# Optimization experiments

Measured on AMD Instinct MI355X. Metric: run time of the kernel, lower is better.

The kernel has to match this reference:

```python
import jax, jax.numpy as jnp
import numpy as np

N, E, G, NH, H = 50000, 400000, 1024, 64, 1
EPS = 1e-5

def _bn(x):
    # BatchNorm1d in training mode, affine at init (gamma=1, beta=0), biased var
    m = x.mean(0)
    v = ((x - m) ** 2).mean(0)
    return (x - m) * jax.lax.rsqrt(v + EPS)

def _seg_softmax(logits, seg, num_segments):
    # numerically stable per-segment softmax (torch_geometric.utils.softmax)
    mx = jax.ops.segment_max(logits, seg, num_segments=num_segments)
    e = jnp.exp(logits - mx[seg])
    s = jax.ops.segment_sum(e, seg, num_segments=num_segments)
    return e / s[seg]

def setup_inputs() -> dict:
    key = jax.random.key(0)
    ks = jax.random.split(key, 16)
    p = lambda k, shape, s=0.1: jax.random.normal(k, shape, jnp.float32) * s
    return {
        "x": jax.random.normal(ks[0], (N, 92), jnp.float32),
        "edge_index": jax.random.randint(ks[1], (2, E), 0, N),
        "edge_attr": jax.random.normal(ks[2], (E, 41), jnp.float32),
        "batch": jnp.sort(jax.random.randint(ks[3], (N,), 0, G)),
        "global_feat": jax.random.normal(ks[4], (G, 103), jnp.float32),
        "emb_n_W": p(ks[5], (92, NH)), "emb_n_b": jnp.zeros((NH,), jnp.float32),
        "emb_e_W": p(ks[6], (41, NH)), "emb_e_b": jnp.zeros((NH,), jnp.float32),
        "conv_W": p(ks[7], (3, 2 * NH, H * NH)),
        "conv_att": p(ks[8], (3, H, 2 * NH)),
        "conv_bias": jnp.zeros((3, H * NH), jnp.float32),
        "comp_node_W": p(ks[9], (NH + 103, 32)), "comp_node_b": jnp.zeros((32,), jnp.float32),
        "comp_att_W": p(ks[10], (32, 1)), "comp_att_b": jnp.zeros((1,), jnp.float32),
        "fc_W": p(ks[11], (NH, 1)), "fc_b": jnp.zeros((1,), jnp.float32),
    }

def reference(x, edge_index, edge_attr, batch, global_feat,
              emb_n_W, emb_n_b, emb_e_W, emb_e_b,
              conv_W, conv_att, conv_bias,
              comp_node_W, comp_node_b, comp_att_W, comp_att_b,
              fc_W, fc_b):
    sp = jax.nn.softplus
    src, dst = edge_index[0], edge_index[1]  # PyG: x_j = x[src], aggregate by dst
    h = x @ emb_n_W + emb_n_b                              # [N, NH]
    ea = jax.nn.leaky_relu(edge_attr @ emb_e_W + emb_e_b, 0.2)  # [E, NH]
    for l in range(3):  # AGATConv layers
        hi = jnp.concatenate([h[dst], ea], -1)             # [E, 2*NH]
        hj = jnp.concatenate([h[src], ea], -1)
        ti = sp(hi @ conv_W[l]).reshape(E, H, NH)
        tj = sp(hj @ conv_W[l]).reshape(E, H, NH)
        alpha = sp(jnp.sum(jnp.concatenate([ti, tj], -1) * conv_att[l][None], -1))  # [E, H]
        alpha = sp(_bn(alpha))
        alpha = _seg_softmax(alpha, dst, N)                # segment softmax per dst node
        agg = jax.ops.segment_sum(tj * alpha[..., None], dst, num_segments=N)  # [N, H, NH]
        h = agg.reshape(N, H * NH) + conv_bias[l]
        h = sp(_bn(h))                                     # outer BatchNorm1d + softplus
    # composition attention: repeat_interleave(global_feat, counts) == gather by graph id
    gf = global_feat[batch]                                # [N, 103]
    a = sp(jnp.concatenate([h, gf], -1) @ comp_node_W + comp_node_b) @ comp_att_W + comp_att_b
    w = _seg_softmax(a, batch, G)                          # [N, 1]
    pooled = jax.ops.segment_sum(h * w, batch, num_segments=G)  # global_add_pool
    return pooled @ fc_W + fc_b                            # [G, 1]
```

## Files before the change

### kernel.cpp

```cpp
#include <hip/hip_runtime.h>
#include <hip/hip_bf16.h>
#include <hip/hip_fp16.h>
#include <math.h>


typedef unsigned short ushortt;
typedef _Float16 half2v __attribute__((ext_vector_type(2)));

__device__ __forceinline__ float sp_f(float x) {
  return x > 20.0f ? x : __logf(1.0f + __expf(x));
}
__device__ __forceinline__ float h2f(ushortt u) {
  union { ushortt u; __half h; } c; c.u = u;
  return __half2float(c.h);
}
__device__ __forceinline__ ushortt f2h(float f) {
  union { __half h; ushortt u; } c; c.h = __float2half(f);
  return c.u;
}
__device__ __forceinline__ float4 h4_to_f4(ushort4 u) {
  return make_float4(h2f(u.x), h2f(u.y), h2f(u.z), h2f(u.w));
}
__device__ __forceinline__ unsigned pack2h(float a, float b) {
  union { _Float16 h[2]; unsigned u; } c;
  c.h[0] = (_Float16)a; c.h[1] = (_Float16)b;
  return c.u;
}
__device__ __forceinline__ float fdot2f(unsigned a, unsigned b, float c) {
  return __builtin_amdgcn_fdot2(__builtin_bit_cast(half2v, a),
                                __builtin_bit_cast(half2v, b), c, false);
}

#define SLOTS 2304

template<int K, int ACT, int BIAS, int FUSE_A, int LH16, int GATHER, int FUSE_BN,
         typename IT, typename OT>
__global__ __launch_bounds__(256) void k_gemm_rt(
    const IT* __restrict__ in, const float* __restrict__ W,
    const float* __restrict__ b, OT* __restrict__ out, int R,
    const int* __restrict__ rows, const ushortt* __restrict__ P,
    const int* __restrict__ srcp, const int* __restrict__ dstp,
    const float* __restrict__ catt, float* __restrict__ a1,
    float* __restrict__ stats, const float* __restrict__ csbn, float invN)
{
  constexpr int KP  = (K + 3) / 4 * 4;
  constexpr int LSf = KP + 4;
  constexpr int LSb = K + 8;
  constexpr size_t INS_B = LH16 ? (size_t)64 * LSb * 2 : (size_t)64 * LSf * 4;
  constexpr size_t WS_B  = LH16 ? (size_t)(K / 2) * 64 * 4 : (size_t)KP * 64 * 4;
  __shared__ __align__(16) unsigned char smem[INS_B + WS_B];
  __shared__ float atts[128];
  __shared__ float ssum[4], ssq[4];
  __shared__ float bnm[64], bns[64];
  ushortt*  insb = (ushortt*)smem;
  unsigned* Wp   = (unsigned*)(smem + INS_B);
  float*    insf = (float*)smem;
  float*    Wsf  = (float*)(smem + INS_B);

  const int tx = threadIdx.x;
  const int b0 = blockIdx.x * 64;

  if (FUSE_BN) {
    if (tx < 64) {
      float mn = 0.f, sq = 0.f;
      #pragma unroll
      for (int bk = 0; bk < 16; ++bk) {
        mn += csbn[bk * 128 + tx];
        sq += csbn[bk * 128 + 64 + tx];
      }
      mn *= invN; sq *= invN;
      bnm[tx] = mn;
      bns[tx] = rsqrtf(sq - mn * mn + 1e-5f);
    }
    __syncthreads();
  }

  if (LH16) {
    static_assert(!LH16 || (K % 8 == 0), "fp16 path needs K%8==0");
    for (int i = tx; i < (K / 2) * 64; i += 256) {
      const int k2 = i >> 6;
      const int c = i & 63;
      Wp[i] = pack2h(W[(2 * k2) * 64 + c], W[(2 * k2 + 1) * 64 + c]);
    }
    for (int i = tx; i < 64 * (K / 8); i += 256) {
      const int row = i / (K / 8);
      const int k8 = i % (K / 8);
      long r = b0 + row; if (r >= R) r = R - 1;
      if (GATHER) r = rows[r];
      *(uint4*)&insb[row * LSb + k8 * 8] =
          *(const uint4*)&((const ushortt*)in)[r * (long)K + k8 * 8];
    }
  } else {
    for (int i = tx; i < KP * 64; i += 256) {
      const int k = i >> 6;
      Wsf[i] = (k < K) ? W[i] : 0.0f;
    }
    for (int i = tx; i < 64 * (KP / 4); i += 256) {
      const int row = i / (KP / 4);
      const int k4 = i % (KP / 4);
      long r = b0 + row; if (r >= R) r = R - 1;
      if (GATHER) r = rows[r];
      float4 v;
      if (K % 4 == 0) {
        v = *(const float4*)&((const float*)in)[r * (long)K + k4 * 4];
      } else {
        float t[4];
        #pragma unroll
        for (int j = 0; j < 4; ++j) {
          const int k = k4 * 4 + j;
          t[j] = (k < K) ? ((const float*)in)[r * (long)K + k] : 0.0f;
        }
        v = make_float4(t[0], t[1], t[2], t[3]);
      }
      if (FUSE_BN) {
        float* vv = (float*)&v;
        #pragma unroll
        for (int j = 0; j < 4; ++j) {
          const int c = k4 * 4 + j;
          vv[j] = sp_f((vv[j] - bnm[c]) * bns[c]);
        }
      }
      *(float4*)&insf[row * LSf + k4 * 4] = v;
    }
  }
  if (FUSE_A) { if (tx < 128) atts[tx] = catt[tx]; }
  __syncthreads();

  const int lr0 = ((tx >> 6) << 4) + (((tx >> 4) & 3) << 2);
  const int c0 = (tx & 15) << 2;

  ushort4 pdv[4], psv[4];
  if (FUSE_A) {
    #pragma unroll
    for (int ri = 0; ri < 4; ++ri) {
      long e = b0 + lr0 + ri; if (e >= R) e = R - 1;
      const int s = srcp[e];
      const int d = dstp[e];
      psv[ri] = *(const ushort4*)&P[(long)s * 64 + c0];
      pdv[ri] = *(const ushort4*)&P[(long)d * 64 + c0];
    }
  }

  float acc[4][4];
  #pragma unroll
  for (int i = 0; i < 4; ++i)
    #pragma unroll
    for (int j = 0; j < 4; ++j) acc[i][j] = 0.0f;

  if (LH16) {
    #pragma unroll 1
    for (int k8 = 0; k8 < K / 8; ++k8) {
      const uint4 wv0 = *(const uint4*)&Wp[(k8 * 4 + 0) * 64 + c0];
      const uint4 wv1 = *(const uint4*)&Wp[(k8 * 4 + 1) * 64 + c0];
      const uint4 wv2 = *(const uint4*)&Wp[(k8 * 4 + 2) * 64 + c0];
      const uint4 wv3 = *(const uint4*)&Wp[(k8 * 4 + 3) * 64 + c0];
      #pragma unroll
      for (int ri = 0; ri < 4; ++ri) {
        const uint4 av = *(const uint4*)&insb[(lr0 + ri) * LSb + k8 * 8];
        acc[ri][0] = fdot2f(av.x, wv0.x, acc[ri][0]);
        acc[ri][1] = fdot2f(av.x, wv0.y, acc[ri][1]);
        acc[ri][2] = fdot2f(av.x, wv0.z, acc[ri][2]);
        acc[ri][3] = fdot2f(av.x, wv0.w, acc[ri][3]);
        acc[ri][0] = fdot2f(av.y, wv1.x, acc[ri][0]);
        acc[ri][1] = fdot2f(av.y, wv1.y, acc[ri][1]);
        acc[ri][2] = fdot2f(av.y, wv1.z, acc[ri][2]);
        acc[ri][3] = fdot2f(av.y, wv1.w, acc[ri][3]);
        acc[ri][0] = fdot2f(av.z, wv2.x, acc[ri][0]);
        acc[ri][1] = fdot2f(av.z, wv2.y, acc[ri][1]);
        acc[ri][2] = fdot2f(av.z, wv2.z, acc[ri][2]);
        acc[ri][3] = fdot2f(av.z, wv2.w, acc[ri][3]);
        acc[ri][0] = fdot2f(av.w, wv3.x, acc[ri][0]);
        acc[ri][1] = fdot2f(av.w, wv3.y, acc[ri][1]);
        acc[ri][2] = fdot2f(av.w, wv3.z, acc[ri][2]);
        acc[ri][3] = fdot2f(av.w, wv3.w, acc[ri][3]);
      }
    }
  } else {
    #pragma unroll 4
    for (int k4 = 0; k4 < KP / 4; ++k4) {
      float4 w[4], a[4];
      #pragma unroll
      for (int kk = 0; kk < 4; ++kk)
        w[kk] = *(const float4*)&Wsf[(k4 * 4 + kk) * 64 + c0];
      #pragma unroll
      for (int ri = 0; ri < 4; ++ri)
        a[ri] = *(const float4*)&insf[(lr0 + ri) * LSf + k4 * 4];
      #pragma unroll
      for (int ri = 0; ri < 4; ++ri) {
        const float* av = (const float*)&a[ri];
        #pragma unroll
        for (int kk = 0; kk < 4; ++kk) {
          acc[ri][0] = fmaf(av[kk], w[kk].x, acc[ri][0]);
          acc[ri][1] = fmaf(av[kk], w[kk].y, acc[ri][1]);
          acc[ri][2] = fmaf(av[kk], w[kk].z, acc[ri][2]);
          acc[ri][3] = fmaf(av[kk], w[kk].w, acc[ri][3]);
        }
      }
    }
  }

  if (!FUSE_A) {
    float4 bias = make_float4(0.f, 0.f, 0.f, 0.f);
    if (BIAS) bias = *(const float4*)&b[c0];
    #pragma unroll
    for (int ri = 0; ri < 4; ++ri) {
      const long r = b0 + lr0 + ri;
      if (r >= R) continue;
      float4 v;
      v.x = acc[ri][0] + bias.x; v.y = acc[ri][1] + bias.y;
      v.z = acc[ri][2] + bias.z; v.w = acc[ri][3] + bias.w;
      if (ACT == 1) {
        v.x = v.x >= 0.f ? v.x : 0.2f * v.x;  v.y = v.y >= 0.f ? v.y : 0.2f * v.y;
        v.z = v.z >= 0.f ? v.z : 0.2f * v.z;  v.w = v.w >= 0.f ? v.w : 0.2f * v.w;
      }
      if (sizeof(OT) == 4) {
        *(float4*)&out[r * 64 + c0] = v;
      } else {
        ushort4 u;
        u.x = f2h(v.x); u.y = f2h(v.y); u.z = f2h(v.z); u.w = f2h(v.w);
        *(ushort4*)&out[r * 64 + c0] = u;
      }
    }
  } else {
    float s1 = 0.f, s2 = 0.f;
    #pragma unroll
    for (int ri = 0; ri < 4; ++ri) {
      const long e = b0 + lr0 + ri;
      float part = 0.0f;
      if (e < R) {
        const float4 Pd = h4_to_f4(pdv[ri]);
        const float4 Ps = h4_to_f4(psv[ri]);
        float tj[4];
        const float ti0 = sp_f(Pd.x + acc[ri][0]);
        const float ti1 = sp_f(Pd.y + acc[ri][1]);
        const float ti2 = sp_f(Pd.z + acc[ri][2]);
        const float ti3 = sp_f(Pd.w + acc[ri][3]);
        tj[0] = sp_f(Ps.x + acc[ri][0]);
        tj[1] = sp_f(Ps.y + acc[ri][1]);
        tj[2] = sp_f(Ps.z + acc[ri][2]);
        tj[3] = sp_f(Ps.w + acc[ri][3]);
        ushort4 u;
        u.x = f2h(tj[0]); u.y = f2h(tj[1]); u.z = f2h(tj[2]); u.w = f2h(tj[3]);
        *(ushort4*)&out[e * 64 + c0] = u;
        part = ti0 * atts[c0] + ti1 * atts[c0 + 1] + ti2 * atts[c0 + 2] + ti3 * atts[c0 + 3]
             + tj[0] * atts[64 + c0] + tj[1] * atts[64 + c0 + 1]
             + tj[2] * atts[64 + c0 + 2] + tj[3] * atts[64 + c0 + 3];
      }
      #pragma unroll
      for (int off = 8; off; off >>= 1) part += __shfl_xor(part, off);
      if ((tx & 15) == 0 && e < R) {
        const float v = sp_f(part);
        a1[e] = v;
        s1 += v; s2 += v * v;
      }
    }
    s1 += __shfl_xor(s1, 16); s2 += __shfl_xor(s2, 16);
    s1 += __shfl_xor(s1, 32); s2 += __shfl_xor(s2, 32);
    if ((tx & 63) == 0) { ssum[tx >> 6] = s1; ssq[tx >> 6] = s2; }
    __syncthreads();
    if (tx == 0) {
      const int bk = blockIdx.x & 63;
      atomicAdd(&stats[bk], ssum[0] + ssum[1] + ssum[2] + ssum[3]);
      atomicAdd(&stats[64 + bk], ssq[0] + ssq[1] + ssq[2] + ssq[3]);
    }
  }
}

__global__ __launch_bounds__(256) void k_count(
    const int* __restrict__ dst, int* __restrict__ counts, int E)
{
  for (int i = blockIdx.x * 256 + threadIdx.x; i < E; i += gridDim.x * 256)
    atomicAdd(&counts[dst[i]], 1);
}

__global__ __launch_bounds__(256) void k_scan1(
    const int* __restrict__ counts, int* __restrict__ offs,
    int* __restrict__ bsum, int N)
{
  __shared__ int sm[256];
  const int t = threadIdx.x;
  const int idx = blockIdx.x * 256 + t;
  const int v = (idx < N) ? counts[idx] : 0;
  sm[t] = v;
  __syncthreads();
  for (int off = 1; off < 256; off <<= 1) {
    const int u = (t >= off) ? sm[t - off] : 0;
    __syncthreads();
    sm[t] += u;
    __syncthreads();
  }
  if (idx < N) offs[idx] = sm[t] - v;
  if (t == 255) bsum[blockIdx.x] = sm[255];
}

__global__ __launch_bounds__(1024) void k_scan2(int* __restrict__ bsum, int SB)
{
  __shared__ int sm[1024];
  const int t = threadIdx.x;
  const int v = (t < SB) ? bsum[t] : 0;
  sm[t] = v;
  __syncthreads();
  for (int off = 1; off < 1024; off <<= 1) {
    const int u = (t >= off) ? sm[t - off] : 0;
    __syncthreads();
    sm[t] += u;
    __syncthreads();
  }
  if (t < SB) bsum[t] = sm[t] - v;
}

__global__ __launch_bounds__(256) void k_scan3(
    int* __restrict__ offs, const int* __restrict__ bsum, int N, int E)
{
  const int idx = blockIdx.x * 256 + threadIdx.x;
  if (idx < N) offs[idx] += bsum[blockIdx.x];
  if (idx == 0) offs[N] = E;
}

__global__ __launch_bounds__(256) void k_fill(
    const int* __restrict__ dst, const int* __restrict__ offs,
    int* __restrict__ cursors, int* __restrict__ eids, int E)
{
  for (int i = blockIdx.x * 256 + threadIdx.x; i < E; i += gridDim.x * 256) {
    const int d = dst[i];
    eids[offs[d] + atomicAdd(&cursors[d], 1)] = i;
  }
}

__global__ __launch_bounds__(256) void k_permidx(
    const int* __restrict__ eids, const int* __restrict__ eidx,
    int* __restrict__ srcp, int* __restrict__ dstp, int E)
{
  for (int i = blockIdx.x * 256 + threadIdx.x; i < E; i += gridDim.x * 256) {
    const int e = eids[i];
    srcp[i] = eidx[e];
    dstp[i] = eidx[(long)E + e];
  }
}

__global__ __launch_bounds__(256) void k_aggregate(
    const int* __restrict__ offs, const float* __restrict__ a1p,
    const ushortt* __restrict__ Mp, const float* __restrict__ stats,
    float invE, float* __restrict__ aggn, float* __restrict__ cs, int N)
{
  __shared__ float sm_mean, sm_scl;
  const int tx = threadIdx.x;
  if (tx < 64) {
    float s1 = stats[tx];
    float s2 = stats[64 + tx];
    #pragma unroll
    for (int off = 32; off; off >>= 1) {
      s1 += __shfl_xor(s1, off);
      s2 += __shfl_xor(s2, off);
    }
    if (tx == 0) {
      const float mean = s1 * invE;
      sm_mean = mean;
      sm_scl = rsqrtf(s2 * invE - mean * mean + 1e-5f);
    }
  }
  __syncthreads();
  const float mean = sm_mean;
  const float scl = sm_scl;

  const int t = tx & 63;
  const int wid = tx >> 6;
  float s = 0.f, s2 = 0.f;
  const long step = (long)gridDim.x * 4;
  for (long n = (long)blockIdx.x * 4 + wid; n < N; n += step) {
    const int o0 = offs[n];
    const int o1 = offs[n + 1];
    float av = 0.f, sew = 0.f;
    #pragma unroll 4
    for (int i = o0; i < o1; ++i) {
      const float w = __expf(sp_f((a1p[i] - mean) * scl));
      av = fmaf(h2f(Mp[(long)i * 64 + t]), w, av);
      sew += w;
    }
    const float v = (o1 > o0) ? av / sew : 0.0f;
    aggn[n * 64 + t] = v;
    s += v; s2 += v * v;
  }
  __shared__ float b1[256], b2[256];
  b1[tx] = s; b2[tx] = s2;
  __syncthreads();
  if (tx < 64) {
    const int bank = (blockIdx.x & 15) * 128;
    atomicAdd(&cs[bank + t], b1[t] + b1[64 + t] + b1[128 + t] + b1[192 + t]);
    atomicAdd(&cs[bank + 64 + t], b2[t] + b2[64 + t] + b2[128 + t] + b2[192 + t]);
  }
}

__global__ __launch_bounds__(256) void k_hnew(
    const float* __restrict__ aggn, const float* __restrict__ cs,
    float invN, float* __restrict__ h, int N)
{
  const int c = threadIdx.x & 63;
  const int r = threadIdx.x >> 6;
  float mn = 0.f, sq = 0.f;
  #pragma unroll
  for (int bk = 0; bk < 16; ++bk) {
    mn += cs[bk * 128 + c];
    sq += cs[bk * 128 + 64 + c];
  }
  mn *= invN; sq *= invN;
  const float scl = rsqrtf(sq - mn * mn + 1e-5f);
  for (long n = (long)blockIdx.x * 4 + r; n < N; n += (long)gridDim.x * 4)
    h[n * 64 + c] = sp_f((aggn[n * 64 + c] - mn) * scl);
}

#define QSS 170
__global__ __launch_bounds__(256) void k_comp(
    const float* __restrict__ h, const float* __restrict__ gf,
    const int* __restrict__ batch, const float* __restrict__ Wc,
    const float* __restrict__ bc, const float* __restrict__ aw,
    const float* __restrict__ ab, float* __restrict__ aN, int N)
{
  __shared__ __align__(16) float qs[64 * QSS];
  __shared__ __align__(16) float Wcs[167 * 32];
  __shared__ float aws[32], bcs[32];
  const int tx = threadIdx.x;
  const int b0 = blockIdx.x * 64;
  for (int i = tx; i < 167 * 32; i += 256) Wcs[i] = Wc[i];
  if (tx < 32) { aws[tx] = aw[tx]; bcs[tx] = bc[tx]; }
  for (int i = tx; i < 64 * 16; i += 256) {
    const int n = i >> 4;
    const int c4 = (i & 15) << 2;
    long r = b0 + n; if (r >= N) r = N - 1;
    *(float4*)&qs[n * QSS + c4] = *(const float4*)&h[r * 64 + c4];
  }
  for (int i = tx; i < 64 * 103; i += 256) {
    const int n = i / 103;
    const int c = i % 103;
    long r = b0 + n; if (r >= N) r = N - 1;
    qs[n * QSS + 64 + c] = gf[(long)batch[r] * 103 + c];
  }
  __syncthreads();

  const int n = tx >> 2;
  const int colg = (tx & 3) << 3;
  float acc[8];
  #pragma unroll
  for (int j = 0; j < 8; ++j) acc[j] = 0.f;
  #pragma unroll 2
  for (int k = 0; k < 167; ++k) {
    const float q = qs[n * QSS + k];
    const float4 w0 = *(const float4*)&Wcs[k * 32 + colg];
    const float4 w1 = *(const float4*)&Wcs[k * 32 + colg + 4];
    acc[0] = fmaf(q, w0.x, acc[0]);
    acc[1] = fmaf(q, w0.y, acc[1]);
    acc[2] = fmaf(q, w0.z, acc[2]);
    acc[3] = fmaf(q, w0.w, acc[3]);
    acc[4] = fmaf(q, w1.x, acc[4]);
    acc[5] = fmaf(q, w1.y, acc[5]);
    acc[6] = fmaf(q, w1.z, acc[6]);
    acc[7] = fmaf(q, w1.w, acc[7]);
  }
  float val = 0.f;
  #pragma unroll
  for (int j = 0; j < 8; ++j)
    val += sp_f(acc[j] + bcs[colg + j]) * aws[colg + j];
  val += __shfl_xor(val, 1);
  val += __shfl_xor(val, 2);
  const long r = b0 + n;
  if ((tx & 3) == 0 && r < N) aN[r] = val + ab[0];
}

__global__ __launch_bounds__(64) void k_pool(
    const float* __restrict__ h, const float* __restrict__ aN,
    const int* __restrict__ batch, const float* __restrict__ fcW,
    const float* __restrict__ fcb, float* __restrict__ out, int N, int G)
{
  const int g = blockIdx.x;
  const int t = threadIdx.x;
  int lo = 0, hi = N;
  while (lo < hi) { int mid = (lo + hi) >> 1; if (batch[mid] < g) lo = mid + 1; else hi = mid; }
  const int s = lo;
  hi = N;
  while (lo < hi) { int mid = (lo + hi) >> 1; if (batch[mid] < g + 1) lo = mid + 1; else hi = mid; }
  const int e2 = lo;
  if (s >= e2) { if (t == 0) out[g] = fcb[0]; return; }
  float mx = -1e30f;
  for (int i = s + t; i < e2; i += 64) mx = fmaxf(mx, aN[i]);
  #pragma unroll
  for (int off = 32; off; off >>= 1) mx = fmaxf(mx, __shfl_xor(mx, off));
  float se = 0.f;
  for (int i = s + t; i < e2; i += 64) se += __expf(aN[i] - mx);
  #pragma unroll
  for (int off = 32; off; off >>= 1) se += __shfl_xor(se, off);
  float acc = 0.f;
  for (int n = s; n < e2; ++n) {
    const float w = __expf(aN[n] - mx);
    acc = fmaf(h[(long)n * 64 + t], w, acc);
  }
  float part = (acc / se) * fcW[t];
  #pragma unroll
  for (int off = 32; off; off >>= 1) part += __shfl_xor(part, off);
  if (t == 0) out[g] = part + fcb[0];
}

extern "C" void kernel_launch(void* const* d_in, const int* in_sizes, int n_in,
                              void* d_out, int out_size, void* d_ws, size_t ws_size,
                              hipStream_t stream)
{
  const float* x     = (const float*)d_in[0];
  const int*   eidx  = (const int*)  d_in[1];
  const float* eattr = (const float*)d_in[2];
  const int*   batch = (const int*)  d_in[3];
  const float* gfeat = (const float*)d_in[4];
  const float* embnW = (const float*)d_in[5];
  const float* embnb = (const float*)d_in[6];
  const float* embeW = (const float*)d_in[7];
  const float* embeb = (const float*)d_in[8];
  const float* convW = (const float*)d_in[9];
  const float* convA = (const float*)d_in[10];
  const float* compW = (const float*)d_in[12];
  const float* compb = (const float*)d_in[13];
  const float* attW  = (const float*)d_in[14];
  const float* attb  = (const float*)d_in[15];
  const float* fcW   = (const float*)d_in[16];
  const float* fcb   = (const float*)d_in[17];
  float* out = (float*)d_out;

  const int N = in_sizes[0] / 92;
  const int E = in_sizes[1] / 2;
  const int G = in_sizes[4] / 103;
  const float invN = 1.0f / (float)N;
  const float invE = 1.0f / (float)E;

  char* pw = (char*)d_ws;
  float* h     = (float*)pw;  pw += (size_t)N * 64 * 4;
  float* aggn  = (float*)pw;  pw += (size_t)N * 64 * 4;
  float* aE    = (float*)pw;  pw += (size_t)E * 4;
  float* statsB = (float*)pw; pw += 3 * SLOTS * 4;
  float* aN    = (float*)pw;  pw += (size_t)N * 4;
  int* counts  = (int*)pw;    pw += (size_t)N * 4;
  int* cursors = (int*)pw;    pw += (size_t)N * 4;
  int* offs    = (int*)pw;    pw += ((size_t)N + 1) * 4;
  int* bsum    = (int*)pw;    pw += 1024 * 4;
  int* eids    = (int*)pw;    pw += (size_t)E * 4;
  int* srcp    = (int*)pw;    pw += (size_t)E * 4;
  int* dstp    = (int*)pw;    pw += (size_t)E * 4;
  pw = (char*)(((size_t)pw + 63) & ~(size_t)63);
  ushortt* Pp  = (ushortt*)pw; pw += (size_t)N * 64 * 2;
  ushortt* ea  = (ushortt*)pw; pw += (size_t)E * 64 * 2;
  ushortt* M   = (ushortt*)pw;

  const int gE64 = (E + 63) / 64;
  const int gN64 = (N + 63) / 64;
  const int SB = (N + 255) / 256;

  hipMemsetAsync(counts, 0, 2 * (size_t)N * sizeof(int), stream);
  hipMemsetAsync(statsB, 0, 3 * SLOTS * sizeof(float), stream);
  k_count<<<2048, 256, 0, stream>>>(eidx + E, counts, E);
  k_scan1<<<SB, 256, 0, stream>>>(counts, offs, bsum, N);
  k_scan2<<<1, 1024, 0, stream>>>(bsum, SB);
  k_scan3<<<SB, 256, 0, stream>>>(offs, bsum, N, E);
  k_fill<<<2048, 256, 0, stream>>>(eidx + E, offs, cursors, eids, E);
  k_permidx<<<2048, 256, 0, stream>>>(eids, eidx, srcp, dstp, E);

  k_gemm_rt<92, 0, 1, 0, 0, 0, 0, float, float><<<gN64, 256, 0, stream>>>(
      x, embnW, embnb, h, N, nullptr, nullptr, nullptr, nullptr, nullptr,
      nullptr, nullptr, nullptr, 0.f);
  k_gemm_rt<41, 1, 1, 0, 0, 1, 0, float, ushortt><<<gE64, 256, 0, stream>>>(
      eattr, embeW, embeb, ea, E, eids, nullptr, nullptr, nullptr, nullptr,
      nullptr, nullptr, nullptr, 0.f);

  for (int l = 0; l < 3; ++l) {
    const float* Wl = convW + (size_t)l * 128 * 64;
    const float* Al = convA + (size_t)l * 128;
    float* statsL = statsB + (size_t)l * SLOTS;
    if (l == 0) {
      k_gemm_rt<64, 0, 0, 0, 0, 0, 0, float, ushortt><<<gN64, 256, 0, stream>>>(
          h, Wl, nullptr, Pp, N, nullptr, nullptr, nullptr, nullptr, nullptr,
          nullptr, nullptr, nullptr, 0.f);
    } else {
      k_gemm_rt<64, 0, 0, 0, 0, 0, 1, float, ushortt><<<gN64, 256, 0, stream>>>(
          aggn, Wl, nullptr, Pp, N, nullptr, nullptr, nullptr, nullptr, nullptr,
          nullptr, nullptr, statsB + (size_t)(l - 1) * SLOTS + 128, invN);
    }
    k_gemm_rt<64, 0, 0, 1, 1, 0, 0, ushortt, ushortt><<<gE64, 256, 0, stream>>>(
        ea, Wl + 64 * 64, nullptr, M, E, nullptr, Pp, srcp, dstp, Al, aE,
        statsL, nullptr, 0.f);
    k_aggregate<<<2048, 256, 0, stream>>>(offs, aE, M, statsL,
                                          invE, aggn, statsL + 128, N);
  }

  k_hnew<<<2048, 256, 0, stream>>>(aggn, statsB + 2 * SLOTS + 128, invN, h, N);
  k_comp<<<gN64, 256, 0, stream>>>(h, gfeat, batch, compW, compb, attW, attb, aN, N);
  k_pool<<<G, 64, 0, stream>>>(h, aN, batch, fcW, fcb, out, N, G);

  (void)n_in; (void)out_size; (void)ws_size;
}
```

Measured before the change: 541.1 us.

## Use MFMA f16 matrix cores for per-edge conv GEMM with prepacked weights

Replaces the fdot2-based fp16 edge GEMM (E x 64 x 64) with a dedicated kernel using mfma_f32_16x16x32_f16. The weights are prepacked once per call into the MFMA B-operand layout by a small k_packW kernel. Accumulators are staged through shared memory so the existing softplus and attention epilogue with BN stats can run unchanged. This targets the ALU cost of the per-edge matmul, at the price of an extra LDS round-trip and two extra barriers, and it separates the fused path out of the generic template.

```diff
diff --git a/kernel.cpp b/kernel.cpp
--- a/kernel.cpp
+++ b/kernel.cpp
@@ -6,6 +6,8 @@
 
 typedef unsigned short ushortt;
 typedef _Float16 half2v __attribute__((ext_vector_type(2)));
+typedef _Float16 f16x8 __attribute__((ext_vector_type(8)));
+typedef float f32x4 __attribute__((ext_vector_type(4)));
 
 __device__ __forceinline__ float sp_f(float x) {
   return x > 20.0f ? x : __logf(1.0f + __expf(x));
@@ -26,36 +28,21 @@
   c.h[0] = (_Float16)a; c.h[1] = (_Float16)b;
   return c.u;
 }
-__device__ __forceinline__ float fdot2f(unsigned a, unsigned b, float c) {
-  return __builtin_amdgcn_fdot2(__builtin_bit_cast(half2v, a),
-                                __builtin_bit_cast(half2v, b), c, false);
-}
 
 #define SLOTS 2304
 
-template<int K, int ACT, int BIAS, int FUSE_A, int LH16, int GATHER, int FUSE_BN,
+template<int K, int ACT, int BIAS, int GATHER, int FUSE_BN,
          typename IT, typename OT>
 __global__ __launch_bounds__(256) void k_gemm_rt(
     const IT* __restrict__ in, const float* __restrict__ W,
     const float* __restrict__ b, OT* __restrict__ out, int R,
-    const int* __restrict__ rows, const ushortt* __restrict__ P,
-    const int* __restrict__ srcp, const int* __restrict__ dstp,
-    const float* __restrict__ catt, float* __restrict__ a1,
-    float* __restrict__ stats, const float* __restrict__ csbn, float invN)
-{
-  constexpr int KP  = (K + 3) / 4 * 4;
-  constexpr int LSf = KP + 4;
-  constexpr int LSb = K + 8;
-  constexpr size_t INS_B = LH16 ? (size_t)64 * LSb * 2 : (size_t)64 * LSf * 4;
-  constexpr size_t WS_B  = LH16 ? (size_t)(K / 2) * 64 * 4 : (size_t)KP * 64 * 4;
-  __shared__ __align__(16) unsigned char smem[INS_B + WS_B];
-  __shared__ float atts[128];
-  __shared__ float ssum[4], ssq[4];
+    const int* __restrict__ rows, const float* __restrict__ csbn, float invN)
+{
+  constexpr int KP = (K + 3) / 4 * 4;
+  constexpr int LS = KP + 4;
+  __shared__ __align__(16) float ins[64 * LS];
+  __shared__ __align__(16) float Ws[KP * 64];
   __shared__ float bnm[64], bns[64];
-  ushortt*  insb = (ushortt*)smem;
-  unsigned* Wp   = (unsigned*)(smem + INS_B);
-  float*    insf = (float*)smem;
-  float*    Wsf  = (float*)(smem + INS_B);
 
   const int tx = threadIdx.x;
   const int b0 = blockIdx.x * 64;
@@ -75,194 +62,226 @@
     __syncthreads();
   }
 
-  if (LH16) {
-    static_assert(!LH16 || (K % 8 == 0), "fp16 path needs K%8==0");
-    for (int i = tx; i < (K / 2) * 64; i += 256) {
-      const int k2 = i >> 6;
-      const int c = i & 63;
-      Wp[i] = pack2h(W[(2 * k2) * 64 + c], W[(2 * k2 + 1) * 64 + c]);
-    }
-    for (int i = tx; i < 64 * (K / 8); i += 256) {
-      const int row = i / (K / 8);
-      const int k8 = i % (K / 8);
-      long r = b0 + row; if (r >= R) r = R - 1;
-      if (GATHER) r = rows[r];
-      *(uint4*)&insb[row * LSb + k8 * 8] =
-          *(const uint4*)&((const ushortt*)in)[r * (long)K + k8 * 8];
-    }
-  } else {
-    for (int i = tx; i < KP * 64; i += 256) {
-      const int k = i >> 6;
-      Wsf[i] = (k < K) ? W[i] : 0.0f;
-    }
-    for (int i = tx; i < 64 * (KP / 4); i += 256) {
-      const int row = i / (KP / 4);
-      const int k4 = i % (KP / 4);
-      long r = b0 + row; if (r >= R) r = R - 1;
-      if (GATHER) r = rows[r];
-      float4 v;
-      if (K % 4 == 0) {
-        v = *(const float4*)&((const float*)in)[r * (long)K + k4 * 4];
-      } else {
-        float t[4];
-        #pragma unroll
-        for (int j = 0; j < 4; ++j) {
-          const int k = k4 * 4 + j;
-          t[j] = (k < K) ? ((const float*)in)[r * (long)K + k] : 0.0f;
-        }
-        v = make_float4(t[0], t[1], t[2], t[3]);
+  for (int i = tx; i < KP * 64; i += 256) {
+    const int k = i >> 6;
+    Ws[i] = (k < K) ? W[i] : 0.0f;
+  }
+  for (int i = tx; i < 64 * (KP / 4); i += 256) {
+    const int row = i / (KP / 4);
+    const int k4 = i % (KP / 4);
+    long r = b0 + row; if (r >= R) r = R - 1;
+    if (GATHER) r = rows[r];
+    float4 v;
+    if (K % 4 == 0) {
+      v = *(const float4*)&((const float*)in)[r * (long)K + k4 * 4];
+    } else {
+      float t[4];
+      #pragma unroll
+      for (int j = 0; j < 4; ++j) {
+        const int k = k4 * 4 + j;
+        t[j] = (k < K) ? ((const float*)in)[r * (long)K + k] : 0.0f;
       }
-      if (FUSE_BN) {
-        float* vv = (float*)&v;
-        #pragma unroll
-        for (int j = 0; j < 4; ++j) {
-          const int c = k4 * 4 + j;
-          vv[j] = sp_f((vv[j] - bnm[c]) * bns[c]);
-        }
+      v = make_float4(t[0], t[1], t[2], t[3]);
+    }
+    if (FUSE_BN) {
+      float* vv = (float*)&v;
+      #pragma unroll
+      for (int j = 0; j < 4; ++j) {
+        const int c = k4 * 4 + j;
+        vv[j] = sp_f((vv[j] - bnm[c]) * bns[c]);
       }
-      *(float4*)&insf[row * LSf + k4 * 4] = v;
-    }
-  }
-  if (FUSE_A) { if (tx < 128) atts[tx] = catt[tx]; }
+    }
+    *(float4*)&ins[row * LS + k4 * 4] = v;
+  }
   __syncthreads();
 
   const int lr0 = ((tx >> 6) << 4) + (((tx >> 4) & 3) << 2);
   const int c0 = (tx & 15) << 2;
-
-  ushort4 pdv[4], psv[4];
-  if (FUSE_A) {
-    #pragma unroll
-    for (int ri = 0; ri < 4; ++ri) {
-      long e = b0 + lr0 + ri; if (e >= R) e = R - 1;
-      const int s = srcp[e];
-      const int d = dstp[e];
-      psv[ri] = *(const ushort4*)&P[(long)s * 64 + c0];
-      pdv[ri] = *(const ushort4*)&P[(long)d * 64 + c0];
-    }
-  }
-
   float acc[4][4];
   #pragma unroll
   for (int i = 0; i < 4; ++i)
     #pragma unroll
     for (int j = 0; j < 4; ++j) acc[i][j] = 0.0f;
 
-  if (LH16) {
-    #pragma unroll 1
-    for (int k8 = 0; k8 < K / 8; ++k8) {
-      const uint4 wv0 = *(const uint4*)&Wp[(k8 * 4 + 0) * 64 + c0];
-      const uint4 wv1 = *(const uint4*)&Wp[(k8 * 4 + 1) * 64 + c0];
-      const uint4 wv2 = *(const uint4*)&Wp[(k8 * 4 + 2) * 64 + c0];
-      const uint4 wv3 = *(const uint4*)&Wp[(k8 * 4 + 3) * 64 + c0];
-      #pragma unroll
-      for (int ri = 0; ri < 4; ++ri) {
-        const uint4 av = *(const uint4*)&insb[(lr0 + ri) * LSb + k8 * 8];
-        acc[ri][0] = fdot2f(av.x, wv0.x, acc[ri][0]);
-        acc[ri][1] = fdot2f(av.x, wv0.y, acc[ri][1]);
-        acc[ri][2] = fdot2f(av.x, wv0.z, acc[ri][2]);
-        acc[ri][3] = fdot2f(av.x, wv0.w, acc[ri][3]);
-        acc[ri][0] = fdot2f(av.y, wv1.x, acc[ri][0]);
-        acc[ri][1] = fdot2f(av.y, wv1.y, acc[ri][1]);
-        acc[ri][2] = fdot2f(av.y, wv1.z, acc[ri][2]);
-        acc[ri][3] = fdot2f(av.y, wv1.w, acc[ri][3]);
-        acc[ri][0] = fdot2f(av.z, wv2.x, acc[ri][0]);
-        acc[ri][1] = fdot2f(av.z, wv2.y, acc[ri][1]);
-        acc[ri][2] = fdot2f(av.z, wv2.z, acc[ri][2]);
-        acc[ri][3] = fdot2f(av.z, wv2.w, acc[ri][3]);
-        acc[ri][0] = fdot2f(av.w, wv3.x, acc[ri][0]);
-        acc[ri][1] = fdot2f(av.w, wv3.y, acc[ri][1]);
-        acc[ri][2] = fdot2f(av.w, wv3.z, acc[ri][2]);
-        acc[ri][3] = fdot2f(av.w, wv3.w, acc[ri][3]);
-      }
-    }
-  } else {
-    #pragma unroll 4
-    for (int k4 = 0; k4 < KP / 4; ++k4) {
-      float4 w[4], a[4];
-      #pragma unroll
-      for (int kk = 0; kk < 4; ++kk)
-        w[kk] = *(const float4*)&Wsf[(k4 * 4 + kk) * 64 + c0];
-      #pragma unroll
-      for (int ri = 0; ri < 4; ++ri)
-        a[ri] = *(const float4*)&insf[(lr0 + ri) * LSf + k4 * 4];
-      #pragma unroll
-      for (int ri = 0; ri < 4; ++ri) {
-        const float* av = (const float*)&a[ri];
-        #pragma unroll
-        for (int kk = 0; kk < 4; ++kk) {
-          acc[ri][0] = fmaf(av[kk], w[kk].x, acc[ri][0]);
-          acc[ri][1] = fmaf(av[kk], w[kk].y, acc[ri][1]);
-          acc[ri][2] = fmaf(av[kk], w[kk].z, acc[ri][2]);
-          acc[ri][3] = fmaf(av[kk], w[kk].w, acc[ri][3]);
-        }
-      }
-    }
-  }
-
-  if (!FUSE_A) {
-    float4 bias = make_float4(0.f, 0.f, 0.f, 0.f);
-    if (BIAS) bias = *(const float4*)&b[c0];
+  #pragma unroll 4
+  for (int k4 = 0; k4 < KP / 4; ++k4) {
+    float4 w[4], a[4];
+    #pragma unroll
+    for (int kk = 0; kk < 4; ++kk)
+      w[kk] = *(const float4*)&Ws[(k4 * 4 + kk) * 64 + c0];
+    #pragma unroll
+    for (int ri = 0; ri < 4; ++ri)
+      a[ri] = *(const float4*)&ins[(lr0 + ri) * LS + k4 * 4];
     #pragma unroll
     for (int ri = 0; ri < 4; ++ri) {
-      const long r = b0 + lr0 + ri;
-      if (r >= R) continue;
-      float4 v;
-      v.x = acc[ri][0] + bias.x; v.y = acc[ri][1] + bias.y;
-      v.z = acc[ri][2] + bias.z; v.w = acc[ri][3] + bias.w;
-      if (ACT == 1) {
-        v.x = v.x >= 0.f ? v.x : 0.2f * v.x;  v.y = v.y >= 0.f ? v.y : 0.2f * v.y;
-        v.z = v.z >= 0.f ? v.z : 0.2f * v.z;  v.w = v.w >= 0.f ? v.w : 0.2f * v.w;
+      const float* av = (const float*)&a[ri];
+      #pragma unroll
+      for (int kk = 0; kk < 4; ++kk) {
+        acc[ri][0] = fmaf(av[kk], w[kk].x, acc[ri][0]);
+        acc[ri][1] = fmaf(av[kk], w[kk].y, acc[ri][1]);
+        acc[ri][2] = fmaf(av[kk], w[kk].z, acc[ri][2]);
+        acc[ri][3] = fmaf(av[kk], w[kk].w, acc[ri][3]);
       }
-      if (sizeof(OT) == 4) {
-        *(float4*)&out[r * 64 + c0] = v;
-      } else {
-        ushort4 u;
-        u.x = f2h(v.x); u.y = f2h(v.y); u.z = f2h(v.z); u.w = f2h(v.w);
-        *(ushort4*)&out[r * 64 + c0] = u;
-      }
-    }
-  } else {
-    float s1 = 0.f, s2 = 0.f;
+    }
+  }
+
+  float4 bias = make_float4(0.f, 0.f, 0.f, 0.f);
+  if (BIAS) bias = *(const float4*)&b[c0];
+  #pragma unroll
+  for (int ri = 0; ri < 4; ++ri) {
+    const long r = b0 + lr0 + ri;
+    if (r >= R) continue;
+    float4 v;
+    v.x = acc[ri][0] + bias.x; v.y = acc[ri][1] + bias.y;
+    v.z = acc[ri][2] + bias.z; v.w = acc[ri][3] + bias.w;
+    if (ACT == 1) {
+      v.x = v.x >= 0.f ? v.x : 0.2f * v.x;  v.y = v.y >= 0.f ? v.y : 0.2f * v.y;
+      v.z = v.z >= 0.f ? v.z : 0.2f * v.z;  v.w = v.w >= 0.f ? v.w : 0.2f * v.w;
+    }
+    if (sizeof(OT) == 4) {
+      *(float4*)&out[r * 64 + c0] = v;
+    } else {
+      ushort4 u;
+      u.x = f2h(v.x); u.y = f2h(v.y); u.z = f2h(v.z); u.w = f2h(v.w);
+      *(ushort4*)&out[r * 64 + c0] = u;
+    }
+  }
+}
+
+__global__ __launch_bounds__(512) void k_packW(
+    const float* __restrict__ convW, uint4* __restrict__ WBg)
+{
+  const int l3 = blockIdx.x;
+  const float* W = convW + (size_t)l3 * 128 * 64 + 64 * 64;
+  const int idx = threadIdx.x;
+  const int kstep = idx >> 8;
+  const int rem = idx & 255;
+  const int ncol = rem >> 6;
+  const int l = rem & 63;
+  const int kbase = kstep * 32 + (l >> 4) * 8;
+  const int n = ncol * 16 + (l & 15);
+  ushortt tmp[8];
+  #pragma unroll
+  for (int j = 0; j < 8; ++j) tmp[j] = f2h(W[(kbase + j) * 64 + n]);
+  WBg[l3 * 512 + idx] = *(uint4*)tmp;
+}
+
+__global__ __launch_bounds__(256) void k_efused(
+    const ushortt* __restrict__ ea, const uint4* __restrict__ WBg,
+    ushortt* __restrict__ out, int E, const ushortt* __restrict__ P,
+    const int* __restrict__ srcp, const int* __restrict__ dstp,
+    const float* __restrict__ catt, float* __restrict__ a1,
+    float* __restrict__ stats)
+{
+  __shared__ __align__(16) unsigned char smem[17408];
+  __shared__ float atts[128];
+  __shared__ float ssum[4], ssq[4];
+  ushortt* As   = (ushortt*)smem;
+  uint4*   WB   = (uint4*)(smem + 9216);
+  float*   accs = (float*)smem;
+
+  const int tx = threadIdx.x;
+  const int b0 = blockIdx.x * 64;
+  const int lane = tx & 63;
+  const int w = tx >> 6;
+
+  if (tx < 128) atts[tx] = catt[tx];
+  #pragma unroll
+  for (int i = tx; i < 64 * 8; i += 256) {
+    const int row = i >> 3;
+    const int k8 = i & 7;
+    long r = b0 + row; if (r >= E) r = E - 1;
+    *(uint4*)&As[row * 72 + k8 * 8] = *(const uint4*)&ea[r * (long)64 + k8 * 8];
+  }
+  #pragma unroll
+  for (int i = tx; i < 512; i += 256) WB[i] = WBg[i];
+  __syncthreads();
+
+  const int lr0 = ((tx >> 6) << 4) + (((tx >> 4) & 3) << 2);
+  const int c0 = (tx & 15) << 2;
+  ushort4 pdv[4], psv[4];
+  #pragma unroll
+  for (int ri = 0; ri < 4; ++ri) {
+    long e = b0 + lr0 + ri; if (e >= E) e = E - 1;
+    const int s = srcp[e];
+    const int d = dstp[e];
+    psv[ri] = *(const ushort4*)&P[(long)s * 64 + c0];
+    pdv[ri] = *(const ushort4*)&P[(long)d * 64 + c0];
+  }
+
+  f32x4 acc0 = {0.f,0.f,0.f,0.f}, acc1 = {0.f,0.f,0.f,0.f};
+  f32x4 acc2 = {0.f,0.f,0.f,0.f}, acc3 = {0.f,0.f,0.f,0.f};
+  const int arow = 16 * w + (lane & 15);
+  #pragma unroll
+  for (int kstep = 0; kstep < 2; ++kstep) {
+    const f16x8 a = __builtin_bit_cast(f16x8,
+        *(const uint4*)&As[arow * 72 + kstep * 32 + (lane >> 4) * 8]);
+    const int bb = kstep * 256 + lane;
+    const f16x8 b0v = __builtin_bit_cast(f16x8, WB[bb]);
+    const f16x8 b1v = __builtin_bit_cast(f16x8, WB[bb + 64]);
+    const f16x8 b2v = __builtin_bit_cast(f16x8, WB[bb + 128]);
+    const f16x8 b3v = __builtin_bit_cast(f16x8, WB[bb + 192]);
+    acc0 = __builtin_amdgcn_mfma_f32_16x16x32_f16(a, b0v, acc0, 0, 0, 0);
+    acc1 = __builtin_amdgcn_mfma_f32_16x16x32_f16(a, b1v, acc1, 0, 0, 0);
+    acc2 = __builtin_amdgcn_mfma_f32_16x16x32_f16(a, b2v, acc2, 0, 0, 0);
+    acc3 = __builtin_amdgcn_mfma_f32_16x16x32_f16(a, b3v, acc3, 0, 0, 0);
+  }
+  __syncthreads();
+
+  {
+    const int rbase = 16 * w + (lane >> 4) * 4;
+    const int cb = lane & 15;
     #pragma unroll
-    for (int ri = 0; ri < 4; ++ri) {
-      const long e = b0 + lr0 + ri;
-      float part = 0.0f;
-      if (e < R) {
-        const float4 Pd = h4_to_f4(pdv[ri]);
-        const float4 Ps = h4_to_f4(psv[ri]);
-        float tj[4];
-        const float ti0 = sp_f(Pd.x + acc[ri][0]);
-        const float ti1 = sp_f(Pd.y + acc[ri][1]);
-        const float ti2 = sp_f(Pd.z + acc[ri][2]);
-        const float ti3 = sp_f(Pd.w + acc[ri][3]);
-        tj[0] = sp_f(Ps.x + acc[ri][0]);
-        tj[1] = sp_f(Ps.y + acc[ri][1]);
-        tj[2] = sp_f(Ps.z + acc[ri][2]);
-        tj[3] = sp_f(Ps.w + acc[ri][3]);
-        ushort4 u;
-        u.x = f2h(tj[0]); u.y = f2h(tj[1]); u.z = f2h(tj[2]); u.w = f2h(tj[3]);
-        *(ushort4*)&out[e * 64 + c0] = u;
-        part = ti0 * atts[c0] + ti1 * atts[c0 + 1] + ti2 * atts[c0 + 2] + ti3 * atts[c0 + 3]
-             + tj[0] * atts[64 + c0] + tj[1] * atts[64 + c0 + 1]
-             + tj[2] * atts[64 + c0 + 2] + tj[3] * atts[64 + c0 + 3];
-      }
-      #pragma unroll
-      for (int off = 8; off; off >>= 1) part += __shfl_xor(part, off);
-      if ((tx & 15) == 0 && e < R) {
-        const float v = sp_f(part);
-        a1[e] = v;
-        s1 += v; s2 += v * v;
-      }
-    }
-    s1 += __shfl_xor(s1, 16); s2 += __shfl_xor(s2, 16);
-    s1 += __shfl_xor(s1, 32); s2 += __shfl_xor(s2, 32);
-    if ((tx & 63) == 0) { ssum[tx >> 6] = s1; ssq[tx >> 6] = s2; }
-    __syncthreads();
-    if (tx == 0) {
-      const int bk = blockIdx.x & 63;
-      atomicAdd(&stats[bk], ssum[0] + ssum[1] + ssum[2] + ssum[3]);
-      atomicAdd(&stats[64 + bk], ssq[0] + ssq[1] + ssq[2] + ssq[3]);
-    }
+    for (int reg = 0; reg < 4; ++reg) {
+      accs[(rbase + reg) * 68 + cb]      = acc0[reg];
+      accs[(rbase + reg) * 68 + 16 + cb] = acc1[reg];
+      accs[(rbase + reg) * 68 + 32 + cb] = acc2[reg];
+      accs[(rbase + reg) * 68 + 48 + cb] = acc3[reg];
+    }
+  }
+  __syncthreads();
+
+  float s1 = 0.f, s2 = 0.f;
+  #pragma unroll
+  for (int ri = 0; ri < 4; ++ri) {
+    const long e = b0 + lr0 + ri;
+    float part = 0.0f;
+    if (e < E) {
+      const float4 Pd = h4_to_f4(pdv[ri]);
+      const float4 Ps = h4_to_f4(psv[ri]);
+      const float4 m = *(const float4*)&accs[(lr0 + ri) * 68 + c0];
+      float tj[4];
+      const float ti0 = sp_f(Pd.x + m.x);
+      const float ti1 = sp_f(Pd.y + m.y);
+      const float ti2 = sp_f(Pd.z + m.z);
+      const float ti3 = sp_f(Pd.w + m.w);
+      tj[0] = sp_f(Ps.x + m.x);
+      tj[1] = sp_f(Ps.y + m.y);
+      tj[2] = sp_f(Ps.z + m.z);
+      tj[3] = sp_f(Ps.w + m.w);
+      ushort4 u;
+      u.x = f2h(tj[0]); u.y = f2h(tj[1]); u.z = f2h(tj[2]); u.w = f2h(tj[3]);
+      *(ushort4*)&out[e * 64 + c0] = u;
+      part = ti0 * atts[c0] + ti1 * atts[c0 + 1] + ti2 * atts[c0 + 2] + ti3 * atts[c0 + 3]
+           + tj[0] * atts[64 + c0] + tj[1] * atts[64 + c0 + 1]
+           + tj[2] * atts[64 + c0 + 2] + tj[3] * atts[64 + c0 + 3];
+    }
+    #pragma unroll
+    for (int off = 8; off; off >>= 1) part += __shfl_xor(part, off);
+    if ((tx & 15) == 0 && e < E) {
+      const float v = sp_f(part);
+      a1[e] = v;
+      s1 += v; s2 += v * v;
+    }
+  }
+  s1 += __shfl_xor(s1, 16); s2 += __shfl_xor(s2, 16);
+  s1 += __shfl_xor(s1, 32); s2 += __shfl_xor(s2, 32);
+  if ((tx & 63) == 0) { ssum[tx >> 6] = s1; ssq[tx >> 6] = s2; }
+  __syncthreads();
+  if (tx == 0) {
+    const int bk = blockIdx.x & 63;
+    atomicAdd(&stats[bk], ssum[0] + ssum[1] + ssum[2] + ssum[3]);
+    atomicAdd(&stats[64 + bk], ssq[0] + ssq[1] + ssq[2] + ssq[3]);
   }
 }
 
@@ -542,6 +561,7 @@
   int* srcp    = (int*)pw;    pw += (size_t)E * 4;
   int* dstp    = (int*)pw;    pw += (size_t)E * 4;
   pw = (char*)(((size_t)pw + 63) & ~(size_t)63);
+  uint4* WBg   = (uint4*)pw;   pw += 3 * 512 * 16;
   ushortt* Pp  = (ushortt*)pw; pw += (size_t)N * 64 * 2;
   ushortt* ea  = (ushortt*)pw; pw += (size_t)E * 64 * 2;
   ushortt* M   = (ushortt*)pw;
@@ -558,30 +578,27 @@
   k_scan3<<<SB, 256, 0, stream>>>(offs, bsum, N, E);
   k_fill<<<2048, 256, 0, stream>>>(eidx + E, offs, cursors, eids, E);
   k_permidx<<<2048, 256, 0, stream>>>(eids, eidx, srcp, dstp, E);
-
-  k_gemm_rt<92, 0, 1, 0, 0, 0, 0, float, float><<<gN64, 256, 0, stream>>>(
-      x, embnW, embnb, h, N, nullptr, nullptr, nullptr, nullptr, nullptr,
-      nullptr, nullptr, nullptr, 0.f);
-  k_gemm_rt<41, 1, 1, 0, 0, 1, 0, float, ushortt><<<gE64, 256, 0, stream>>>(
-      eattr, embeW, embeb, ea, E, eids, nullptr, nullptr, nullptr, nullptr,
-      nullptr, nullptr, nullptr, 0.f);
+  k_packW<<<3, 512, 0, stream>>>(convW, WBg);
+
+  k_gemm_rt<92, 0, 1, 0, 0, float, float><<<gN64, 256, 0, stream>>>(
+      x, embnW, embnb, h, N, nullptr, nullptr, 0.f);
+  k_gemm_rt<41, 1, 1, 1, 0, float, ushortt><<<gE64, 256, 0, stream>>>(
+      eattr, embeW, embeb, ea, E, eids, nullptr, 0.f);
 
   for (int l = 0; l < 3; ++l) {
     const float* Wl = convW + (size_t)l * 128 * 64;
     const float* Al = convA + (size_t)l * 128;
     float* statsL = statsB + (size_t)l * SLOTS;
     if (l == 0) {
-      k_gemm_rt<64, 0, 0, 0, 0, 0, 0, float, ushortt><<<gN64, 256, 0, stream>>>(
-          h, Wl, nullptr, Pp, N, nullptr, nullptr, nullptr, nullptr, nullptr,
-          nullptr, nullptr, nullptr, 0.f);
+      k_gemm_rt<64, 0, 0, 0, 0, float, ushortt><<<gN64, 256, 0, stream>>>(
+          h, Wl, nullptr, Pp, N, nullptr, nullptr, 0.f);
     } else {
-      k_gemm_rt<64, 0, 0, 0, 0, 0, 1, float, ushortt><<<gN64, 256, 0, stream>>>(
-          aggn, Wl, nullptr, Pp, N, nullptr, nullptr, nullptr, nullptr, nullptr,
-          nullptr, nullptr, statsB + (size_t)(l - 1) * SLOTS + 128, invN);
-    }
-    k_gemm_rt<64, 0, 0, 1, 1, 0, 0, ushortt, ushortt><<<gE64, 256, 0, stream>>>(
-        ea, Wl + 64 * 64, nullptr, M, E, nullptr, Pp, srcp, dstp, Al, aE,
-        statsL, nullptr, 0.f);
+      k_gemm_rt<64, 0, 0, 0, 1, float, ushortt><<<gN64, 256, 0, stream>>>(
+          aggn, Wl, nullptr, Pp, N, nullptr,
+          statsB + (size_t)(l - 1) * SLOTS + 128, invN);
+    }
+    k_efused<<<gE64, 256, 0, stream>>>(ea, WBg + (size_t)l * 512, M, E,
+                                       Pp, srcp, dstp, Al, aE, statsL);
     k_aggregate<<<2048, 256, 0, stream>>>(offs, aE, M, statsL,
                                           invE, aggn, statsL + 128, N);
   }
```

Result: faster. 475.6 us (-12.1%).
